# Kernel optimization log

Measured on AMD Instinct MI355X. Metric: run time of the kernel, lower is better.

Reference implementation:

```python
import jax, jax.numpy as jnp
from jax import lax
import numpy as np


def setup_inputs() -> dict:
    key = jax.random.key(0)
    kx, = jax.random.split(key, 1)
    B, T = 4096, 4096
    x = jax.random.normal(kx, (B, T), dtype=jnp.float32)
    omega_log = jnp.asarray(0.0, dtype=jnp.float32)
    alpha_log = jnp.asarray(0.0, dtype=jnp.float32)
    beta_log = jnp.asarray(0.0, dtype=jnp.float32)
    return {"x": x, "omega_log": omega_log, "alpha_log": alpha_log, "beta_log": beta_log}


def reference(x, omega_log, alpha_log, beta_log):
    # x: [B, T]
    ea = jnp.exp(alpha_log)
    eb = jnp.exp(beta_log)
    denom = 1.0 + ea + eb
    omega = jnp.exp(omega_log)
    alpha = ea / denom
    beta = eb / denom

    # initial variance: unbiased sample variance over time (torch.var default ddof=1)
    s0 = jnp.var(x, axis=1, ddof=1)  # [B]

    xsq = jnp.swapaxes(x[:, :-1] ** 2, 0, 1)  # [T-1, B]

    def step(s_prev, x2_t):
        s_t = omega + alpha * x2_t + beta * s_prev
        return s_t, s_t

    _, rest = lax.scan(step, s0, xsq)  # rest: [T-1, B]
    sigma2 = jnp.concatenate([s0[None, :], rest], axis=0)  # [T, B]
    return jnp.sqrt(jnp.swapaxes(sigma2, 0, 1))  # [B, T]
```

## Files before the change

kernel.cpp:

```cpp
#include <hip/hip_runtime.h>
#include <math.h>

#define B_ROWS 4096
#define T_COLS 4096
#define NTHREADS 256
#define CHUNK 16
#define NWAVES (NTHREADS / 64)

__device__ __forceinline__ float rfl(float v) {
    return __int_as_float(__builtin_amdgcn_readfirstlane(__float_as_int(v)));
}

__global__ __launch_bounds__(NTHREADS) void garch_fused(
    const float* __restrict__ x,
    const float* __restrict__ p_omega_log,
    const float* __restrict__ p_alpha_log,
    const float* __restrict__ p_beta_log,
    float* __restrict__ out)
{
    __shared__ float wA[NWAVES], wB[NWAVES], rSum[NWAVES], rSsq[NWAVES];

    const int t    = threadIdx.x;
    const int lane = t & 63;
    const int wv   = t >> 6;
    const long rbase = (long)blockIdx.x * T_COLS;

    float ea_p = expf(p_alpha_log[0]);
    float eb_p = expf(p_beta_log[0]);
    float denom = 1.0f + ea_p + eb_p;
    float omega = rfl(expf(p_omega_log[0]));
    float alpha = rfl(ea_p / denom);
    float beta  = rfl(eb_p / denom);

    float bpow[CHUNK + 1];
    bpow[0] = 1.0f;
#pragma unroll
    for (int j = 1; j <= CHUNK; ++j) bpow[j] = bpow[j - 1] * beta;

    const float4* xv = reinterpret_cast<const float4*>(x + rbase + (long)CHUNK * t);
    float4 v0 = xv[0], v1 = xv[1], v2 = xv[2], v3 = xv[3];
    float xr[CHUNK] = { v0.x, v0.y, v0.z, v0.w,  v1.x, v1.y, v1.z, v1.w,
                        v2.x, v2.y, v2.z, v2.w,  v3.x, v3.y, v3.z, v3.w };

    float prev = __shfl_up(xr[CHUNK - 1], 1);
    if (lane == 0) prev = (t > 0) ? x[rbase + (long)CHUNK * t - 1] : 0.0f;

    float sum = 0.0f, ssq = 0.0f;
#pragma unroll
    for (int i = 0; i < CHUNK; ++i) { sum += xr[i]; ssq = fmaf(xr[i], xr[i], ssq); }

    float Z[CHUNK];
    float z;
    if (t > 0) { z = fmaf(alpha, prev * prev, omega); Z[0] = z; }
    else       { z = 0.0f;                            Z[0] = 0.0f; }
#pragma unroll
    for (int i = 0; i < CHUNK - 1; ++i) {
        z = fmaf(beta, z, fmaf(alpha, xr[i] * xr[i], omega));
        Z[i + 1] = z;
    }
    float bpart = z;
    float apart = (t == 0) ? bpow[15] : bpow[16];

    float s1 = sum, s2 = ssq;
#pragma unroll
    for (int d = 32; d > 0; d >>= 1) {
        s1 += __shfl_xor(s1, d);
        s2 += __shfl_xor(s2, d);
    }

    float ia = apart, ib = bpart;
#pragma unroll
    for (int d = 1; d < 64; d <<= 1) {
        float pa = __shfl_up(ia, d);
        float pb = __shfl_up(ib, d);
        if (lane >= d) { ib = fmaf(ia, pb, ib); ia = ia * pa; }
    }

    if (lane == 0)  { rSum[wv] = s1; rSsq[wv] = s2; }
    if (lane == 63) { wA[wv] = ia;   wB[wv] = ib;  }
    __syncthreads();

    float tsum = rSum[0] + rSum[1] + rSum[2] + rSum[3];
    float tssq = rSsq[0] + rSsq[1] + rSsq[2] + rSsq[3];
    float s0 = (tssq - tsum * tsum * (1.0f / T_COLS)) * (1.0f / (T_COLS - 1));
    s0 = fmaxf(s0, 0.0f);

    float sw = s0;
#pragma unroll
    for (int w = 0; w < NWAVES - 1; ++w)
        if (w < wv) sw = fmaf(wA[w], sw, wB[w]);

    float pea = __shfl_up(ia, 1);
    float peb = __shfl_up(ib, 1);
    if (lane == 0) { pea = 1.0f; peb = 0.0f; }
    float s = fmaf(pea, sw, peb);

    float4* ov = reinterpret_cast<float4*>(out + rbase + (long)CHUNK * t);
    if (t == 0) {
        float4 o;
        o.x = __builtin_amdgcn_sqrtf(s);
        o.y = __builtin_amdgcn_sqrtf(fmaf(bpow[1], s, Z[1]));
        o.z = __builtin_amdgcn_sqrtf(fmaf(bpow[2], s, Z[2]));
        o.w = __builtin_amdgcn_sqrtf(fmaf(bpow[3], s, Z[3]));
        ov[0] = o;
#pragma unroll
        for (int k = 1; k < 4; ++k) {
            float4 q;
            q.x = __builtin_amdgcn_sqrtf(fmaf(bpow[4 * k + 0], s, Z[4 * k + 0]));
            q.y = __builtin_amdgcn_sqrtf(fmaf(bpow[4 * k + 1], s, Z[4 * k + 1]));
            q.z = __builtin_amdgcn_sqrtf(fmaf(bpow[4 * k + 2], s, Z[4 * k + 2]));
            q.w = __builtin_amdgcn_sqrtf(fmaf(bpow[4 * k + 3], s, Z[4 * k + 3]));
            ov[k] = q;
        }
    } else {
#pragma unroll
        for (int k = 0; k < 4; ++k) {
            float4 q;
            q.x = __builtin_amdgcn_sqrtf(fmaf(bpow[4 * k + 1], s, Z[4 * k + 0]));
            q.y = __builtin_amdgcn_sqrtf(fmaf(bpow[4 * k + 2], s, Z[4 * k + 1]));
            q.z = __builtin_amdgcn_sqrtf(fmaf(bpow[4 * k + 3], s, Z[4 * k + 2]));
            q.w = __builtin_amdgcn_sqrtf(fmaf(bpow[4 * k + 4], s, Z[4 * k + 3]));
            ov[k] = q;
        }
    }
}

extern "C" void kernel_launch(void* const* d_in, const int* in_sizes, int n_in,
                              void* d_out, int out_size, void* d_ws, size_t ws_size,
                              hipStream_t stream) {
    const float* x         = (const float*)d_in[0];
    const float* omega_log = (const float*)d_in[1];
    const float* alpha_log = (const float*)d_in[2];
    const float* beta_log  = (const float*)d_in[3];
    float* out = (float*)d_out;

    garch_fused<<<B_ROWS, NTHREADS, 0, stream>>>(x, omega_log, alpha_log, beta_log, out);
}
```

Before: 123.1 us.

## Use 1024 threads per row with one float4 per thread

Each block now uses 1024 threads, and each thread processes 4 elements instead of 16. Consecutive threads therefore load and store adjacent float4s, which coalesces global memory access. The cross-wave prefix combine grows from 4 to 16 waves, and that serial loop is no longer unrolled. This adds more shuffle-scan and sync overhead per element, and the larger blocks may reduce scheduling flexibility.

```diff
diff --git a/kernel.cpp b/kernel.cpp
--- a/kernel.cpp
+++ b/kernel.cpp
@@ -3,8 +3,7 @@
 
 #define B_ROWS 4096
 #define T_COLS 4096
-#define NTHREADS 256
-#define CHUNK 16
+#define NTHREADS 1024
 #define NWAVES (NTHREADS / 64)
 
 __device__ __forceinline__ float rfl(float v) {
@@ -31,35 +30,30 @@
     float omega = rfl(expf(p_omega_log[0]));
     float alpha = rfl(ea_p / denom);
     float beta  = rfl(eb_p / denom);
+    float b1 = beta, b2 = b1 * beta, b3 = b2 * beta, b4 = b3 * beta;
 
-    float bpow[CHUNK + 1];
-    bpow[0] = 1.0f;
-#pragma unroll
-    for (int j = 1; j <= CHUNK; ++j) bpow[j] = bpow[j - 1] * beta;
+    const float4* xv = reinterpret_cast<const float4*>(x + rbase);
+    float4 v = xv[t];
 
-    const float4* xv = reinterpret_cast<const float4*>(x + rbase + (long)CHUNK * t);
-    float4 v0 = xv[0], v1 = xv[1], v2 = xv[2], v3 = xv[3];
-    float xr[CHUNK] = { v0.x, v0.y, v0.z, v0.w,  v1.x, v1.y, v1.z, v1.w,
-                        v2.x, v2.y, v2.z, v2.w,  v3.x, v3.y, v3.z, v3.w };
+    float prev = __shfl_up(v.w, 1);
+    if (lane == 0) prev = (t > 0) ? x[rbase + 4 * t - 1] : 0.0f;
 
-    float prev = __shfl_up(xr[CHUNK - 1], 1);
-    if (lane == 0) prev = (t > 0) ? x[rbase + (long)CHUNK * t - 1] : 0.0f;
+    float sum = (v.x + v.y) + (v.z + v.w);
+    float ssq = fmaf(v.x, v.x, fmaf(v.y, v.y, fmaf(v.z, v.z, v.w * v.w)));
 
-    float sum = 0.0f, ssq = 0.0f;
-#pragma unroll
-    for (int i = 0; i < CHUNK; ++i) { sum += xr[i]; ssq = fmaf(xr[i], xr[i], ssq); }
-
-    float Z[CHUNK];
-    float z;
-    if (t > 0) { z = fmaf(alpha, prev * prev, omega); Z[0] = z; }
-    else       { z = 0.0f;                            Z[0] = 0.0f; }
-#pragma unroll
-    for (int i = 0; i < CHUNK - 1; ++i) {
-        z = fmaf(beta, z, fmaf(alpha, xr[i] * xr[i], omega));
-        Z[i + 1] = z;
+    float Z0, Z1, Z2, Z3, apart;
+    if (t > 0) {
+        Z0 = fmaf(alpha, prev * prev, omega);
+        Z1 = fmaf(beta, Z0, fmaf(alpha, v.x * v.x, omega));
+        apart = b4;
+    } else {
+        Z0 = 0.0f;
+        Z1 = fmaf(alpha, v.x * v.x, omega);
+        apart = b3;
     }
-    float bpart = z;
-    float apart = (t == 0) ? bpow[15] : bpow[16];
+    Z2 = fmaf(beta, Z1, fmaf(alpha, v.y * v.y, omega));
+    Z3 = fmaf(beta, Z2, fmaf(alpha, v.z * v.z, omega));
+    float bpart = Z3;
 
     float s1 = sum, s2 = ssq;
 #pragma unroll
@@ -80,49 +74,34 @@
     if (lane == 63) { wA[wv] = ia;   wB[wv] = ib;  }
     __syncthreads();
 
-    float tsum = rSum[0] + rSum[1] + rSum[2] + rSum[3];
-    float tssq = rSsq[0] + rSsq[1] + rSsq[2] + rSsq[3];
+    float tsum = 0.0f, tssq = 0.0f;
+#pragma unroll
+    for (int w = 0; w < NWAVES; ++w) { tsum += rSum[w]; tssq += rSsq[w]; }
     float s0 = (tssq - tsum * tsum * (1.0f / T_COLS)) * (1.0f / (T_COLS - 1));
     s0 = fmaxf(s0, 0.0f);
 
     float sw = s0;
-#pragma unroll
-    for (int w = 0; w < NWAVES - 1; ++w)
-        if (w < wv) sw = fmaf(wA[w], sw, wB[w]);
+    for (int w = 0; w < wv; ++w) sw = fmaf(wA[w], sw, wB[w]);
 
     float pea = __shfl_up(ia, 1);
     float peb = __shfl_up(ib, 1);
     if (lane == 0) { pea = 1.0f; peb = 0.0f; }
     float s = fmaf(pea, sw, peb);
 
-    float4* ov = reinterpret_cast<float4*>(out + rbase + (long)CHUNK * t);
+    float4 o;
     if (t == 0) {
-        float4 o;
         o.x = __builtin_amdgcn_sqrtf(s);
-        o.y = __builtin_amdgcn_sqrtf(fmaf(bpow[1], s, Z[1]));
-        o.z = __builtin_amdgcn_sqrtf(fmaf(bpow[2], s, Z[2]));
-        o.w = __builtin_amdgcn_sqrtf(fmaf(bpow[3], s, Z[3]));
-        ov[0] = o;
-#pragma unroll
-        for (int k = 1; k < 4; ++k) {
-            float4 q;
-            q.x = __builtin_amdgcn_sqrtf(fmaf(bpow[4 * k + 0], s, Z[4 * k + 0]));
-            q.y = __builtin_amdgcn_sqrtf(fmaf(bpow[4 * k + 1], s, Z[4 * k + 1]));
-            q.z = __builtin_amdgcn_sqrtf(fmaf(bpow[4 * k + 2], s, Z[4 * k + 2]));
-            q.w = __builtin_amdgcn_sqrtf(fmaf(bpow[4 * k + 3], s, Z[4 * k + 3]));
-            ov[k] = q;
-        }
+        o.y = __builtin_amdgcn_sqrtf(fmaf(b1, s, Z1));
+        o.z = __builtin_amdgcn_sqrtf(fmaf(b2, s, Z2));
+        o.w = __builtin_amdgcn_sqrtf(fmaf(b3, s, Z3));
     } else {
-#pragma unroll
-        for (int k = 0; k < 4; ++k) {
-            float4 q;
-            q.x = __builtin_amdgcn_sqrtf(fmaf(bpow[4 * k + 1], s, Z[4 * k + 0]));
-            q.y = __builtin_amdgcn_sqrtf(fmaf(bpow[4 * k + 2], s, Z[4 * k + 1]));
-            q.z = __builtin_amdgcn_sqrtf(fmaf(bpow[4 * k + 3], s, Z[4 * k + 2]));
-            q.w = __builtin_amdgcn_sqrtf(fmaf(bpow[4 * k + 4], s, Z[4 * k + 3]));
-            ov[k] = q;
-        }
+        o.x = __builtin_amdgcn_sqrtf(fmaf(b1, s, Z0));
+        o.y = __builtin_amdgcn_sqrtf(fmaf(b2, s, Z1));
+        o.z = __builtin_amdgcn_sqrtf(fmaf(b3, s, Z2));
+        o.w = __builtin_amdgcn_sqrtf(fmaf(b4, s, Z3));
     }
+    float4* ov = reinterpret_cast<float4*>(out + rbase);
+    ov[t] = o;
 }
 
 extern "C" void kernel_launch(void* const* d_in, const int* in_sizes, int n_in,
```

Result: slower. 129.3 us (+5.0%).
